# Kernel tuning notes

Measured on AMD Instinct MI355X. Metric: run time of the kernel, lower is better.

## Reference

```python
import jax, jax.numpy as jnp
import numpy as np

# Pair indices for combinations(16, 2, with_replacement=True): (i, j) with i <= j,
# lexicographic order -> identical to np.triu_indices(16).
_II, _JJ = np.triu_indices(16)


def setup_inputs() -> dict:
    key = jax.random.key(0)
    k1, k2, k3 = jax.random.split(key, 3)
    B, M, K = 32, 16, 32
    params = jax.random.normal(k1, (B, M, 2, K, 2), dtype=jnp.float32)
    # knots: strictly increasing per spatial dimension -> sort uniform samples
    knots = jnp.sort(jax.random.uniform(k2, (K, 2), dtype=jnp.float32), axis=0) * K
    integral_coeffs = jax.random.normal(k3, (K - 1, K - 1, 136), dtype=jnp.float32) * 0.1
    return {"params": params, "knots": knots, "integral_coeffs": integral_coeffs}


def _hermite_coeffs(params, knots):
    """Cubic Hermite spline coefficients per interval, in local coords (x - x_i).

    params: [B, M, 2, K, 2] (value, derivative per knot), knots: [K, 2].
    Returns [B, M, 2, K-1, 4] = (c0, c1, c2, c3).
    """
    y = params[..., 0]   # [B, M, 2, K]
    dy = params[..., 1]
    h = (knots[1:] - knots[:-1]).T  # [2, K-1], broadcasts against [B, M, 2, K-1]
    y0, y1 = y[..., :-1], y[..., 1:]
    d0, d1 = dy[..., :-1], dy[..., 1:]
    c0 = y0
    c1 = d0
    c2 = 3.0 * (y1 - y0) / (h * h) - (2.0 * d0 + d1) / h
    c3 = 2.0 * (y0 - y1) / (h * h * h) + (d0 + d1) / (h * h)
    return jnp.stack([c0, c1, c2, c3], axis=-1)  # [B, M, 2, K-1, 4]


def reference(params, knots, integral_coeffs):
    # Spline coefficients for every (batch, mixture, dim) component.
    poly = _hermite_coeffs(params, knots)            # [B, M, 2, Kc, 4]
    B, M, _, Kc, _ = poly.shape
    cx = poly[:, :, 0]                               # [B, M, Kc, 4]
    cy = poly[:, :, 1]                               # [B, M, Kc, 4]
    # meshgrid + cartesian_prod == outer product of the two cubic coefficient
    # vectors per 2D grid cell -> 16 monomial coeffs of the product polynomial.
    G = jnp.einsum('bmia,bmjc->bmijac', cx, cy).reshape(B, M, Kc, Kc, 16)
    # Squared polynomial: pairwise products over the 16 coeffs (i <= j, 136 pairs),
    # weighted by precomputed per-cell integral coefficients and summed.
    P = G[..., _II] * G[..., _JJ]                    # [B, M, Kc, Kc, 136]
    Z = jnp.sum(P * integral_coeffs, axis=-1)        # [B, M, Kc, Kc]
    return poly, Z
```

## Files before the change

### kernel.cpp

```cpp
#include <hip/hip_runtime.h>


#define BM_TOTAL 512
#define KC 31
#define NPAIR 136
#define POLY_ITEMS 31744
#define POLY_FLOATS 126976
#define Z_STRIDE 961

__global__ __launch_bounds__(256) void spline_sq2d_kernel(
    const float* __restrict__ params,
    const float* __restrict__ knots,
    const float* __restrict__ coeffs,
    float* __restrict__ out)
{
    const int tid = threadIdx.x;
    const int blk = blockIdx.x;

    if (blk < (POLY_ITEMS / 256)) {
        const int gid = blk * 256 + tid;
        const int k   = gid % KC;
        const int rem = gid / KC;
        const int dim = rem & 1;
        const float* p = params + (rem * 32 + k) * 2;
        const float2 v0 = *(const float2*)(p);
        const float2 v1 = *(const float2*)(p + 2);
        const float y0 = v0.x, d0 = v0.y, y1 = v1.x, d1 = v1.y;
        const float h  = knots[(k + 1) * 2 + dim] - knots[k * 2 + dim];
        const float c2 = 3.0f * (y1 - y0) / (h * h) - (2.0f * d0 + d1) / h;
        const float c3 = 2.0f * (y0 - y1) / (h * h * h) + (d0 + d1) / (h * h);
        float4 o; o.x = y0; o.y = d0; o.z = c2; o.w = c3;
        ((float4*)out)[gid] = o;
    }

    __shared__ float cf[NPAIR];
    if (tid < NPAIR) cf[tid] = coeffs[blk * NPAIR + tid];
    __syncthreads();

    const int i = blk / KC;
    const int j = blk % KC;

    const float hx = knots[(i + 1) * 2 + 0] - knots[i * 2 + 0];
    const float hy = knots[(j + 1) * 2 + 1] - knots[j * 2 + 1];
    const float ihx = 1.0f / hx, ihx2 = ihx * ihx, ihx3 = ihx2 * ihx;
    const float ihy = 1.0f / hy, ihy2 = ihy * ihy, ihy3 = ihy2 * ihy;

    float* __restrict__ zout = out + POLY_FLOATS;

    for (int bm = tid; bm < BM_TOTAL; bm += 256) {
        const float* px = params + (bm * 64 + i) * 2;
        const float2 a0 = *(const float2*)px;
        const float2 a1 = *(const float2*)(px + 2);
        const float* py = params + (bm * 64 + 32 + j) * 2;
        const float2 b0 = *(const float2*)py;
        const float2 b1 = *(const float2*)(py + 2);

        float cx[4], cy[4];
        cx[0] = a0.x;
        cx[1] = a0.y;
        cx[2] = 3.0f * (a1.x - a0.x) * ihx2 - (2.0f * a0.y + a1.y) * ihx;
        cx[3] = 2.0f * (a0.x - a1.x) * ihx3 + (a0.y + a1.y) * ihx2;
        cy[0] = b0.x;
        cy[1] = b0.y;
        cy[2] = 3.0f * (b1.x - b0.x) * ihy2 - (2.0f * b0.y + b1.y) * ihy;
        cy[3] = 2.0f * (b0.x - b1.x) * ihy3 + (b0.y + b1.y) * ihy2;

        float g[16];
        #pragma unroll
        for (int a = 0; a < 4; ++a)
            #pragma unroll
            for (int c = 0; c < 4; ++c)
                g[a * 4 + c] = cx[a] * cy[c];

        float sum = 0.0f;
        int p = 0;
        #pragma unroll
        for (int u = 0; u < 16; ++u) {
            const float gu = g[u];
            #pragma unroll
            for (int v = u; v < 16; ++v) {
                sum = fmaf(gu * g[v], cf[p], sum);
                ++p;
            }
        }

        zout[bm * Z_STRIDE + blk] = sum;
    }
}

extern "C" void kernel_launch(void* const* d_in, const int* in_sizes, int n_in,
                              void* d_out, int out_size, void* d_ws, size_t ws_size,
                              hipStream_t stream) {
    const float* params = (const float*)d_in[0];
    const float* knots  = (const float*)d_in[1];
    const float* coeffs = (const float*)d_in[2];
    float* out = (float*)d_out;
    (void)in_sizes; (void)n_in; (void)out_size; (void)d_ws; (void)ws_size;

    spline_sq2d_kernel<<<KC * KC, 256, 0, stream>>>(params, knots, coeffs, out);
}
```

Baseline: 68.16 us.

## Factor squared-polynomial integral into separable 10x10 form via coefficient prepass

A prepass kernel folds the 136 pair coefficients per cell into a 10x10 matrix indexed by symmetric x-pairs and y-pairs. The main kernel then forms 10 symmetric products per axis and evaluates a bilinear form, instead of building 16 outer-product terms and 136 pair products. Each thread now handles both batch-mixture items explicitly, with their loads hoisted and interleaved. This cuts arithmetic per output, but adds a second launch, a workspace round trip, and coefficient reads from global memory rather than shared memory.

Measured after the change: 68.56 us. No clear change (+0.6%).

```diff
diff --git a/kernel.cpp b/kernel.cpp
--- a/kernel.cpp
+++ b/kernel.cpp
@@ -7,11 +7,36 @@
 #define POLY_ITEMS 31744
 #define POLY_FLOATS 126976
 #define Z_STRIDE 961
+#define D_STRIDE 128
 
-__global__ __launch_bounds__(256) void spline_sq2d_kernel(
+__global__ __launch_bounds__(128) void spline_prepass(
+    const float* __restrict__ coeffs,
+    float* __restrict__ ws)
+{
+    const int t = threadIdx.x;
+    const int blk = blockIdx.x;
+    if (t >= 100) return;
+    const int al = t / 10, be = t % 10;
+    const int TA [10] = {0,0,0,0,1,1,1,2,2,3};
+    const int TA2[10] = {0,1,2,3,1,2,3,2,3,3};
+    const int a = TA[al], a2 = TA2[al];
+    const int c = TA[be], c2 = TA2[be];
+    const float* C = coeffs + blk * NPAIR;
+    auto pidx = [](int u, int v) { return u * 16 - (u * (u - 1)) / 2 + (v - u); };
+    float val;
+    if (a == a2) {
+        val = C[pidx(4 * a + c, 4 * a + c2)];
+    } else {
+        val = C[pidx(4 * a + c, 4 * a2 + c2)];
+        if (c != c2) val += C[pidx(4 * a + c2, 4 * a2 + c)];
+    }
+    ws[blk * D_STRIDE + t] = val;
+}
+
+__global__ __launch_bounds__(256) void spline_main(
     const float* __restrict__ params,
     const float* __restrict__ knots,
-    const float* __restrict__ coeffs,
+    const float* __restrict__ ws,
     float* __restrict__ out)
 {
     const int tid = threadIdx.x;
@@ -33,10 +58,6 @@
         ((float4*)out)[gid] = o;
     }
 
-    __shared__ float cf[NPAIR];
-    if (tid < NPAIR) cf[tid] = coeffs[blk * NPAIR + tid];
-    __syncthreads();
-
     const int i = blk / KC;
     const int j = blk % KC;
 
@@ -45,47 +66,67 @@
     const float ihx = 1.0f / hx, ihx2 = ihx * ihx, ihx3 = ihx2 * ihx;
     const float ihy = 1.0f / hy, ihy2 = ihy * ihy, ihy3 = ihy2 * ihy;
 
-    float* __restrict__ zout = out + POLY_FLOATS;
+    const int bm0 = tid, bm1 = tid + 256;
+    const float* px0 = params + (bm0 * 64 + i) * 2;
+    const float2 a00 = *(const float2*)px0;
+    const float2 a01 = *(const float2*)(px0 + 2);
+    const float* py0 = params + (bm0 * 64 + 32 + j) * 2;
+    const float2 b00 = *(const float2*)py0;
+    const float2 b01 = *(const float2*)(py0 + 2);
+    const float* px1 = params + (bm1 * 64 + i) * 2;
+    const float2 a10 = *(const float2*)px1;
+    const float2 a11 = *(const float2*)(px1 + 2);
+    const float* py1 = params + (bm1 * 64 + 32 + j) * 2;
+    const float2 b10 = *(const float2*)py1;
+    const float2 b11 = *(const float2*)(py1 + 2);
 
-    for (int bm = tid; bm < BM_TOTAL; bm += 256) {
-        const float* px = params + (bm * 64 + i) * 2;
-        const float2 a0 = *(const float2*)px;
-        const float2 a1 = *(const float2*)(px + 2);
-        const float* py = params + (bm * 64 + 32 + j) * 2;
-        const float2 b0 = *(const float2*)py;
-        const float2 b1 = *(const float2*)(py + 2);
+    float cx0[4], cy0[4], cx1[4], cy1[4];
+    cx0[0] = a00.x; cx0[1] = a00.y;
+    cx0[2] = 3.0f * (a01.x - a00.x) * ihx2 - (2.0f * a00.y + a01.y) * ihx;
+    cx0[3] = 2.0f * (a00.x - a01.x) * ihx3 + (a00.y + a01.y) * ihx2;
+    cy0[0] = b00.x; cy0[1] = b00.y;
+    cy0[2] = 3.0f * (b01.x - b00.x) * ihy2 - (2.0f * b00.y + b01.y) * ihy;
+    cy0[3] = 2.0f * (b00.x - b01.x) * ihy3 + (b00.y + b01.y) * ihy2;
+    cx1[0] = a10.x; cx1[1] = a10.y;
+    cx1[2] = 3.0f * (a11.x - a10.x) * ihx2 - (2.0f * a10.y + a11.y) * ihx;
+    cx1[3] = 2.0f * (a10.x - a11.x) * ihx3 + (a10.y + a11.y) * ihx2;
+    cy1[0] = b10.x; cy1[1] = b10.y;
+    cy1[2] = 3.0f * (b11.x - b10.x) * ihy2 - (2.0f * b10.y + b11.y) * ihy;
+    cy1[3] = 2.0f * (b10.x - b11.x) * ihy3 + (b10.y + b11.y) * ihy2;
 
-        float cx[4], cy[4];
-        cx[0] = a0.x;
-        cx[1] = a0.y;
-        cx[2] = 3.0f * (a1.x - a0.x) * ihx2 - (2.0f * a0.y + a1.y) * ihx;
-        cx[3] = 2.0f * (a0.x - a1.x) * ihx3 + (a0.y + a1.y) * ihx2;
-        cy[0] = b0.x;
-        cy[1] = b0.y;
-        cy[2] = 3.0f * (b1.x - b0.x) * ihy2 - (2.0f * b0.y + b1.y) * ihy;
-        cy[3] = 2.0f * (b0.x - b1.x) * ihy3 + (b0.y + b1.y) * ihy2;
-
-        float g[16];
+    float X0[10], Y0[10], X1[10], Y1[10];
+    {
+        int q = 0;
         #pragma unroll
         for (int a = 0; a < 4; ++a)
             #pragma unroll
-            for (int c = 0; c < 4; ++c)
-                g[a * 4 + c] = cx[a] * cy[c];
+            for (int a2 = a; a2 < 4; ++a2) {
+                X0[q] = cx0[a] * cx0[a2];
+                X1[q] = cx1[a] * cx1[a2];
+                Y0[q] = cy0[a] * cy0[a2];
+                Y1[q] = cy1[a] * cy1[a2];
+                ++q;
+            }
+    }
 
-        float sum = 0.0f;
-        int p = 0;
+    const float* __restrict__ Dp = ws + blk * D_STRIDE;
+    float s0 = 0.0f, s1 = 0.0f;
+    #pragma unroll
+    for (int al = 0; al < 10; ++al) {
+        float w0 = 0.0f, w1 = 0.0f;
         #pragma unroll
-        for (int u = 0; u < 16; ++u) {
-            const float gu = g[u];
-            #pragma unroll
-            for (int v = u; v < 16; ++v) {
-                sum = fmaf(gu * g[v], cf[p], sum);
-                ++p;
-            }
+        for (int be = 0; be < 10; ++be) {
+            const float d = Dp[al * 10 + be];
+            w0 = fmaf(d, Y0[be], w0);
+            w1 = fmaf(d, Y1[be], w1);
         }
+        s0 = fmaf(X0[al], w0, s0);
+        s1 = fmaf(X1[al], w1, s1);
+    }
 
-        zout[bm * Z_STRIDE + blk] = sum;
-    }
+    float* __restrict__ zout = out + POLY_FLOATS;
+    zout[bm0 * Z_STRIDE + blk] = s0;
+    zout[bm1 * Z_STRIDE + blk] = s1;
 }
 
 extern "C" void kernel_launch(void* const* d_in, const int* in_sizes, int n_in,
@@ -95,7 +136,9 @@
     const float* knots  = (const float*)d_in[1];
     const float* coeffs = (const float*)d_in[2];
     float* out = (float*)d_out;
-    (void)in_sizes; (void)n_in; (void)out_size; (void)d_ws; (void)ws_size;
+    float* ws  = (float*)d_ws;
+    (void)in_sizes; (void)n_in; (void)out_size; (void)ws_size;
 
-    spline_sq2d_kernel<<<KC * KC, 256, 0, stream>>>(params, knots, coeffs, out);
+    spline_prepass<<<KC * KC, 128, 0, stream>>>(coeffs, ws);
+    spline_main<<<KC * KC, 256, 0, stream>>>(params, knots, ws, out);
 }
```
